# Performance work log

Measured on AMD Instinct MI355X. Metric: run time of the kernel, lower is better.

Reference implementation:

```python
import jax, jax.numpy as jnp
import numpy as np

T, B = 50, 512
S, A, BEL, H, E, M = 256, 32, 1024, 1024, 1024, 256
MIN_STD = 0.1


def setup_inputs() -> dict:
    key = jax.random.key(0)
    ks = jax.random.split(key, 24)
    def rn(k, shape, scale=1.0):
        return jax.random.normal(k, shape, dtype=jnp.float32) * scale
    w = 0.05  # weight init scale
    return {
        "prev_state": rn(ks[0], (B, S)),
        "actions": rn(ks[1], (T, B, A)),
        "prev_belief": rn(ks[2], (B, BEL)),
        "observations": rn(ks[3], (T, B, E)),
        "nonterminals": jnp.ones((T, B, 1), dtype=jnp.float32),
        "map_embeddings": rn(ks[4], (T, B, M)),
        "map_embeddings_post": rn(ks[5], (T, B, M)),
        "noise_prior": rn(ks[6], (T, B, S)),
        "noise_post": rn(ks[7], (T, B, S)),
        "W_sa": rn(ks[8], (BEL, S + A + M), w), "b_sa": jnp.zeros((BEL,), jnp.float32),
        "W_ih": rn(ks[9], (3 * BEL, BEL), w), "b_ih": jnp.zeros((3 * BEL,), jnp.float32),
        "W_hh": rn(ks[10], (3 * BEL, BEL), w), "b_hh": jnp.zeros((3 * BEL,), jnp.float32),
        "W_bp": rn(ks[11], (H, BEL), w), "b_bp": jnp.zeros((H,), jnp.float32),
        "W_sp": rn(ks[12], (2 * S, H), w), "b_sp": jnp.zeros((2 * S,), jnp.float32),
        "W_bq": rn(ks[13], (H, BEL + E + M), w), "b_bq": jnp.zeros((H,), jnp.float32),
        "W_sq": rn(ks[14], (2 * S, H), w), "b_sq": jnp.zeros((2 * S,), jnp.float32),
    }


def reference(prev_state, actions, prev_belief, observations, nonterminals,
              map_embeddings, map_embeddings_post, noise_prior, noise_post,
              W_sa, b_sa, W_ih, b_ih, W_hh, b_hh,
              W_bp, b_bp, W_sp, b_sp, W_bq, b_bq, W_sq, b_sq):
    relu = jax.nn.relu
    def lin(x, W, b):
        return x @ W.T + b

    def gru(x, h):  # torch.nn.GRUCell math
        gi = x @ W_ih.T + b_ih
        gh = h @ W_hh.T + b_hh
        i_r, i_z, i_n = jnp.split(gi, 3, axis=1)
        h_r, h_z, h_n = jnp.split(gh, 3, axis=1)
        r = jax.nn.sigmoid(i_r + h_r)
        z = jax.nn.sigmoid(i_z + h_z)
        n = jnp.tanh(i_n + r * h_n)
        return (1.0 - z) * n + z * h

    def std(raw):
        return jnp.minimum(jax.nn.softplus(raw) + MIN_STD, 5.0)

    def step(carry, xs):
        belief, post_state = carry
        a, obs, nt, me, mp, np_, nq = xs
        s = post_state * nt
        hid = relu(lin(jnp.concatenate([s, a, me], axis=1), W_sa, b_sa))
        belief = gru(hid, belief)
        # prior p(z_t | h_t)
        hp = relu(lin(belief, W_bp, b_bp))
        p_mean, p_raw = jnp.split(lin(hp, W_sp, b_sp), 2, axis=1)
        p_std = std(p_raw)
        p_state = p_mean + p_std * np_
        # posterior q(z_t | h_t, e_t, m_t)
        hq = relu(lin(jnp.concatenate([belief, obs, mp], axis=1), W_bq, b_bq))
        q_mean, q_raw = jnp.split(lin(hq, W_sq, b_sq), 2, axis=1)
        q_std = std(q_raw)
        q_state = q_mean + q_std * nq
        return (belief, q_state), (belief, p_state, p_mean, p_std, q_state, q_mean, q_std)

    _, outs = jax.lax.scan(
        step, (prev_belief, prev_state),
        (actions, observations, nonterminals, map_embeddings,
         map_embeddings_post, noise_prior, noise_post))
    return outs  # 7 arrays, each (T, B, *)
```

## Files before the change

### kernel.cpp

```cpp
#include <hip/hip_runtime.h>
#include <hip/hip_bf16.h>

#define NT 50
#define NB 512
#define SD 256
#define BD 1024
#define HD 1024
#define ED 1024
#define MD 256
#define NBLK 512
#define PGSZ (1024 * 256)
#define K1BIG 0x40000000
#define WPRE_OFF 49152

typedef __attribute__((ext_vector_type(8))) short bf16x8;
typedef __attribute__((ext_vector_type(4))) float f32x4;

__device__ __forceinline__ void gload_lds16(const void* g, void* l) {
  __builtin_amdgcn_global_load_lds(
      (const __attribute__((address_space(1))) void*)g,
      (__attribute__((address_space(3))) void*)l, 16, 0, 0);
}
__device__ __forceinline__ void gload_lds16_sc0(const void* g, void* l) {
  __builtin_amdgcn_global_load_lds(
      (const __attribute__((address_space(1))) void*)g,
      (__attribute__((address_space(3))) void*)l, 16, 0, 1);
}

__device__ __forceinline__ void aload16(const void* a, f32x4* r) {
  asm volatile("global_load_dwordx4 %0, %1, off sc0" : "=&v"(*r) : "v"(a) : "memory");
}
__device__ __forceinline__ void aload4(const void* a, float* r) {
  asm volatile("global_load_dword %0, %1, off sc0" : "=&v"(*r) : "v"(a) : "memory");
}
__device__ __forceinline__ void aload2(const void* a, unsigned* r) {
  asm volatile("global_load_ushort %0, %1, off sc0" : "=&v"(*r) : "v"(a) : "memory");
}
#define VMWAIT(N)                                        \
  asm volatile("s_waitcnt vmcnt(" #N ")" ::: "memory");  \
  __builtin_amdgcn_sched_barrier(0);

__device__ __forceinline__ void astore16(void* g, f32x4 v) {
  asm volatile("global_store_dwordx4 %0, %1, off sc0" :: "v"(g), "v"(v) : "memory");
}
__device__ __forceinline__ void astore4(void* g, float v) {
  asm volatile("global_store_dword %0, %1, off sc0" :: "v"(g), "v"(v) : "memory");
}
__device__ __forceinline__ void astore2(void* g, unsigned v) {
  asm volatile("global_store_short %0, %1, off sc0" :: "v"(g), "v"(v) : "memory");
}
__device__ __forceinline__ void ntstore4(void* g, float v) {
  asm volatile("global_store_dword %0, %1, off nt" :: "v"(g), "v"(v) : "memory");
}

__device__ __forceinline__ float sigmoidf_(float x) { return 1.0f / (1.0f + __expf(-x)); }
__device__ __forceinline__ float softplusf_(float x) {
  return (x > 0.0f) ? (x + log1pf(__expf(-x))) : log1pf(__expf(x));
}
__device__ __forceinline__ unsigned short bfb(float x) {
  __hip_bfloat16 h = __float2bfloat16(x);
  return __builtin_bit_cast(unsigned short, h);
}
__device__ __forceinline__ float b2f(unsigned short u) {
  __hip_bfloat16 h = __builtin_bit_cast(__hip_bfloat16, u);
  return __bfloat162float(h);
}

__device__ __forceinline__ void wpre_issue(const __hip_bfloat16* W, int ldw,
                                           char* lds, int tid) {
  const int w = tid >> 6, lane = tid & 63;
  const __hip_bfloat16* wrow = W + (size_t)lane * ldw;
  char* wpre = lds + WPRE_OFF;
#pragma unroll
  for (int c = 0; c < 3; ++c) {
    gload_lds16(wrow + (c << 6) + (2 * w) * 8, wpre + c * 8192 + (2 * w) * 1024);
    gload_lds16(wrow + (c << 6) + (2 * w + 1) * 8, wpre + c * 8192 + (2 * w + 1) * 1024);
  }
}

__device__ __forceinline__ void xbar_pf(unsigned* cnt, int inst, int xcd, int nx,
                                        const __hip_bfloat16* nextW, int nextLdw,
                                        char* lds, int tid) {
  asm volatile("s_waitcnt vmcnt(0) lgkmcnt(0)" ::: "memory");
  __syncthreads();
  unsigned* c = cnt + 256 + (size_t)(inst * 8 + xcd) * 16;
  if (tid == 0)
    __hip_atomic_fetch_add(c, 1u, __ATOMIC_RELAXED, __HIP_MEMORY_SCOPE_AGENT);
  if (nextW) wpre_issue(nextW, nextLdw, lds, tid);
  if (tid == 0) {
    while (__hip_atomic_load(c, __ATOMIC_RELAXED, __HIP_MEMORY_SCOPE_AGENT) < (unsigned)nx)
      __builtin_amdgcn_s_sleep(2);
  }
  __syncthreads();
}

__device__ __noinline__ void gemm64(
    int EPI, char* lds, bool pre,
    const __hip_bfloat16* __restrict__ A1, int lda1,
    const __hip_bfloat16* __restrict__ A2, int lda2, int K1,
    const __hip_bfloat16* __restrict__ Wr, int ldw, int nIter,
    const float* __restrict__ bias, const void* __restrict__ Cadd,
    __hip_bfloat16* __restrict__ Cb, int ldc, int m0) {
  const int tid = threadIdx.x;
  const int lane = tid & 63, w = tid >> 6;
  const int wr = w >> 1, wc = w & 1;
  f32x4 acc[2][2] = {};
  const __hip_bfloat16* a1r = A1 + (size_t)(m0 + lane) * lda1;
  const __hip_bfloat16* a2r = A2 ? (A2 + (size_t)(m0 + lane) * lda2) : a1r;
  const __hip_bfloat16* wrow = Wr + (size_t)lane * ldw;
  char* wpre = lds + WPRE_OFF;

  auto aissue = [&](int it) {
    const int k0 = it << 6;
    char* la = lds + (size_t)(it % 3) * 16384;
    const __hip_bfloat16* as = (k0 < K1) ? (a1r + k0) : (a2r + (k0 - K1));
    gload_lds16_sc0(as + (2 * w) * 8, la + (2 * w) * 1024);
    gload_lds16_sc0(as + (2 * w + 1) * 8, la + (2 * w + 1) * 1024);
  };
  auto stageAW = [&](int it) {
    const int k0 = it << 6;
    char* la = lds + (size_t)(it % 3) * 16384;
    char* lb = la + 8192;
    const __hip_bfloat16* as = (k0 < K1) ? (a1r + k0) : (a2r + (k0 - K1));
    gload_lds16_sc0(as + (2 * w) * 8, la + (2 * w) * 1024);
    gload_lds16_sc0(as + (2 * w + 1) * 8, la + (2 * w + 1) * 1024);
    gload_lds16(wrow + k0 + (2 * w) * 8, lb + (2 * w) * 1024);
    gload_lds16(wrow + k0 + (2 * w + 1) * 8, lb + (2 * w + 1) * 1024);
  };

  __syncthreads();
  if (!pre) wpre_issue(Wr, ldw, lds, tid);
  aissue(0);
  aissue(1);
  aissue(2);
  VMWAIT(4)
  __builtin_amdgcn_s_barrier();
  __builtin_amdgcn_sched_barrier(0);

  const int kq = lane >> 4, r15 = lane & 15;
  for (int i = 0; i < nIter; ++i) {
    const char* la = lds + (size_t)(i % 3) * 16384;
    const char* lb = (i < 3) ? (wpre + (size_t)i * 8192) : (la + 8192);
#pragma unroll
    for (int s = 0; s < 2; ++s) {
      bf16x8 af[2], bfr[2];
#pragma unroll
      for (int m = 0; m < 2; ++m)
        af[m] = *(const bf16x8*)(la + (size_t)((s * 4 + kq) * 64 + wr * 32 + m * 16 + r15) * 16);
#pragma unroll
      for (int n = 0; n < 2; ++n)
        bfr[n] = *(const bf16x8*)(lb + (size_t)((s * 4 + kq) * 64 + wc * 32 + n * 16 + r15) * 16);
#pragma unroll
      for (int m = 0; m < 2; ++m)
#pragma unroll
        for (int n = 0; n < 2; ++n)
          acc[m][n] = __builtin_amdgcn_mfma_f32_16x16x32_bf16(af[m], bfr[n], acc[m][n], 0, 0, 0);
    }
    if (i + 1 < nIter) {
      if (i == 0) {
        VMWAIT(2)
      } else if (i + 2 < nIter) {
        VMWAIT(4)
      } else {
        VMWAIT(0)
      }
      __builtin_amdgcn_s_barrier();
      __builtin_amdgcn_sched_barrier(0);
      if (i + 3 < nIter) stageAW(i + 3);
    }
  }

  const int rg = lane >> 4;
  unsigned adu[2][2][4];
  if (EPI == 5) {
#pragma unroll
    for (int m = 0; m < 2; ++m)
#pragma unroll
      for (int n = 0; n < 2; ++n) {
        const int col = wc * 32 + n * 16 + r15;
#pragma unroll
        for (int i2 = 0; i2 < 4; ++i2) {
          const int row = m0 + wr * 32 + m * 16 + rg * 4 + i2;
          aload2((const unsigned short*)Cadd + (size_t)row * ldc + col, &adu[m][n][i2]);
        }
      }
    VMWAIT(0)
  }
#pragma unroll
  for (int m = 0; m < 2; ++m) {
#pragma unroll
    for (int n = 0; n < 2; ++n) {
      const int col = wc * 32 + n * 16 + r15;
      const float bv = bias ? bias[col] : 0.0f;
#pragma unroll
      for (int i2 = 0; i2 < 4; ++i2) {
        const int row = m0 + wr * 32 + m * 16 + rg * 4 + i2;
        float v = acc[m][n][i2] + bv;
        if (EPI == 5) v += b2f((unsigned short)adu[m][n][i2]);
        if (EPI != 4) v = v > 0.0f ? v : 0.0f;
        astore2(Cb + (size_t)row * ldc + col, (unsigned)bfb(v));
      }
    }
  }
}

__device__ __noinline__ void gemm_gru(
    char* lds, const __hip_bfloat16* __restrict__ Wih3,
    const __hip_bfloat16* __restrict__ Whh3,
    const float* __restrict__ b_ih, const float* __restrict__ b_hh,
    const __hip_bfloat16* __restrict__ hid, const __hip_bfloat16* __restrict__ belR,
    __hip_bfloat16* __restrict__ belW, float* __restrict__ outT, int n, int m0) {
  const int tid = threadIdx.x;
  const int lane = tid & 63, w = tid >> 6;
  f32x4 agi[3] = {}, agh[3] = {};
  const __hip_bfloat16* hrow = hid + (size_t)(m0 + lane) * BD;
  const __hip_bfloat16* brow = belR + (size_t)(m0 + lane) * BD;
  const int wln = (lane < 48) ? lane : 47;
  const __hip_bfloat16* wirow = Wih3 + (size_t)(n * 48 + wln) * BD;
  const __hip_bfloat16* whrow = Whh3 + (size_t)(n * 48 + wln) * BD;

  auto stage = [&](int it) {
    const int k0 = it << 5;
    char* buf = lds + (size_t)(it % 3) * 16384;
    gload_lds16_sc0(hrow + k0 + w * 8, buf + w * 1024);
    gload_lds16_sc0(brow + k0 + w * 8, buf + 4096 + w * 1024);
    gload_lds16(wirow + k0 + w * 8, buf + 8192 + w * 1024);
    gload_lds16(whrow + k0 + w * 8, buf + 12288 + w * 1024);
  };

  __syncthreads();
  stage(0);
  stage(1);
  VMWAIT(4)
  __builtin_amdgcn_s_barrier();
  __builtin_amdgcn_sched_barrier(0);

  const int kq = lane >> 4, r15 = lane & 15;
  for (int i = 0; i < 32; ++i) {
    if (i + 2 < 32) stage(i + 2);
    const char* buf = lds + (size_t)(i % 3) * 16384;
    bf16x8 ah = *(const bf16x8*)(buf + (size_t)(kq * 64 + w * 16 + r15) * 16);
    bf16x8 ab = *(const bf16x8*)(buf + 4096 + (size_t)(kq * 64 + w * 16 + r15) * 16);
#pragma unroll
    for (int g = 0; g < 3; ++g) {
      bf16x8 wi = *(const bf16x8*)(buf + 8192 + (size_t)(kq * 64 + g * 16 + r15) * 16);
      bf16x8 wh = *(const bf16x8*)(buf + 12288 + (size_t)(kq * 64 + g * 16 + r15) * 16);
      agi[g] = __builtin_amdgcn_mfma_f32_16x16x32_bf16(ah, wi, agi[g], 0, 0, 0);
      agh[g] = __builtin_amdgcn_mfma_f32_16x16x32_bf16(ab, wh, agh[g], 0, 0, 0);
    }
    if (i + 1 < 32) {
      if (i + 2 < 32) {
        VMWAIT(4)
      } else {
        VMWAIT(0)
      }
      __builtin_amdgcn_s_barrier();
      __builtin_amdgcn_sched_barrier(0);
    }
  }

  const int rg = lane >> 4;
  const int unit = n * 16 + r15;
  const int rowb = m0 + w * 16 + rg * 4;
  const float bir = b_ih[unit], biz = b_ih[1024 + unit], bin = b_ih[2048 + unit];
  const float bhr = b_hh[unit], bhz = b_hh[1024 + unit], bhn = b_hh[2048 + unit];
  unsigned hp4[4];
#pragma unroll
  for (int i = 0; i < 4; ++i)
    aload2(belR + (size_t)(rowb + i) * BD + unit, &hp4[i]);
  VMWAIT(0)
#pragma unroll
  for (int i = 0; i < 4; ++i) {
    const int row = rowb + i;
    float r_ = sigmoidf_((agi[0][i] + bir) + (agh[0][i] + bhr));
    float z_ = sigmoidf_((agi[1][i] + biz) + (agh[1][i] + bhz));
    float n_ = tanhf((agi[2][i] + bin) + r_ * (agh[2][i] + bhn));
    float hv = b2f((unsigned short)hp4[i]);
    float bel = (1.0f - z_) * n_ + z_ * hv;
    ntstore4(outT + (size_t)row * BD + unit, bel);
    astore2(belW + (size_t)row * BD + unit, (unsigned)bfb(bel));
  }
}

__device__ __noinline__ void gemm_head64(
    char* lds, bool pre, const __hip_bfloat16* __restrict__ A,
    const __hip_bfloat16* __restrict__ Wr, const float* __restrict__ bias,
    const float* __restrict__ noise, float* __restrict__ st_o, float* __restrict__ mn_o,
    float* __restrict__ sd_o, const float* __restrict__ ntn,
    __hip_bfloat16* __restrict__ sprev, int isq, int n0, int m0) {
  const int tid = threadIdx.x;
  const int lane = tid & 63, w = tid >> 6;
  const int wr = w >> 1, wc = w & 1;
  f32x4 acc[2][2] = {};
  const __hip_bfloat16* ar = A + (size_t)(m0 + lane) * BD;
  const __hip_bfloat16* wrow = Wr + (size_t)lane * BD;
  char* wpre = lds + WPRE_OFF;

  auto aissue = [&](int it) {
    const int k0 = it << 6;
    char* la = lds + (size_t)(it % 3) * 16384;
    gload_lds16_sc0(ar + k0 + (2 * w) * 8, la + (2 * w) * 1024);
    gload_lds16_sc0(ar + k0 + (2 * w + 1) * 8, la + (2 * w + 1) * 1024);
  };
  auto stageAW = [&](int it) {
    const int k0 = it << 6;
    char* la = lds + (size_t)(it % 3) * 16384;
    char* lb = la + 8192;
    gload_lds16_sc0(ar + k0 + (2 * w) * 8, la + (2 * w) * 1024);
    gload_lds16_sc0(ar + k0 + (2 * w + 1) * 8, la + (2 * w + 1) * 1024);
    gload_lds16(wrow + k0 + (2 * w) * 8, lb + (2 * w) * 1024);
    gload_lds16(wrow + k0 + (2 * w + 1) * 8, lb + (2 * w + 1) * 1024);
  };

  __syncthreads();
  if (!pre) wpre_issue(Wr, BD, lds, tid);
  aissue(0);
  aissue(1);
  aissue(2);
  VMWAIT(4)
  __builtin_amdgcn_s_barrier();
  __builtin_amdgcn_sched_barrier(0);

  const int kq = lane >> 4, r15 = lane & 15;
  for (int i = 0; i < 16; ++i) {
    const char* la = lds + (size_t)(i % 3) * 16384;
    const char* lb = (i < 3) ? (wpre + (size_t)i * 8192) : (la + 8192);
#pragma unroll
    for (int s = 0; s < 2; ++s) {
      bf16x8 af[2], bfr[2];
#pragma unroll
      for (int m = 0; m < 2; ++m)
        af[m] = *(const bf16x8*)(la + (size_t)((s * 4 + kq) * 64 + wr * 32 + m * 16 + r15) * 16);
#pragma unroll
      for (int n = 0; n < 2; ++n)
        bfr[n] = *(const bf16x8*)(lb + (size_t)((s * 4 + kq) * 64 + wc * 32 + n * 16 + r15) * 16);
#pragma unroll
      for (int m = 0; m < 2; ++m)
#pragma unroll
        for (int n = 0; n < 2; ++n)
          acc[m][n] = __builtin_amdgcn_mfma_f32_16x16x32_bf16(af[m], bfr[n], acc[m][n], 0, 0, 0);
    }
    if (i + 1 < 16) {
      if (i == 0) {
        VMWAIT(2)
      } else if (i + 2 < 16) {
        VMWAIT(4)
      } else {
        VMWAIT(0)
      }
      __builtin_amdgcn_s_barrier();
      __builtin_amdgcn_sched_barrier(0);
      if (i + 3 < 16) stageAW(i + 3);
    }
  }

  const int rg = lane >> 4;
  const bool even = (r15 & 1) == 0;
#pragma unroll
  for (int m = 0; m < 2; ++m) {
#pragma unroll
    for (int n = 0; n < 2; ++n) {
      const int col = n0 + wc * 32 + n * 16 + r15;
      const int j = col >> 1;
      const float bv = bias[col];
#pragma unroll
      for (int i2 = 0; i2 < 4; ++i2) {
        const int row = m0 + wr * 32 + m * 16 + rg * 4 + i2;
        float v = acc[m][n][i2] + bv;
        float partner = __shfl_xor(v, 1);
        float mean = even ? v : partner;
        float raw = even ? partner : v;
        float sd = fminf(softplusf_(raw) + 0.1f, 5.0f);
        const size_t o = (size_t)row * SD + j;
        if (even) {
          float st = mean + sd * noise[o];
          ntstore4(mn_o + o, mean);
          ntstore4(st_o + o, st);
          if (isq) astore2(sprev + o, (unsigned)bfb(st * ntn[row]));
        } else {
          ntstore4(sd_o + o, sd);
        }
      }
    }
  }
}

struct Args {
  const float *prev_state, *actions, *prev_belief, *observations, *nonterminals,
      *me, *mp, *noise_p, *noise_q,
      *W_sa, *b_sa, *W_ih, *b_ih, *W_hh, *b_hh,
      *W_bp, *b_bp, *W_sp, *b_sp, *W_bq, *b_bq, *W_sq, *b_sq;
  float* out;
  unsigned* cnt;
  __hip_bfloat16 *Wsa, *Wih3, *Whh3, *Wbp, *Wbq, *Wsp, *Wsq;
  __hip_bfloat16 *actme, *obsall, *hqall, *sprev, *belA, *belB, *hid, *hpb, *hqb;
  float *bsp_ro, *bsq_ro;
};

__global__ __launch_bounds__(256) void prep(Args P) {
  const int gtid = blockIdx.x * 256 + threadIdx.x;
  for (int i = gtid; i < BD * 576; i += PGSZ) {
    int r = i / 576, k = i - r * 576;
    P.Wsa[i] = __float2bfloat16(k < 544 ? P.W_sa[(size_t)r * 544 + k] : 0.0f);
  }
  for (int i = gtid; i < 3 * BD * BD; i += PGSZ) {
    int rp = i >> 10, k = i & 1023;
    int n = rp / 48, rem = rp - n * 48, g = rem >> 4, u = rem & 15;
    size_t src = (size_t)(g * 1024 + n * 16 + u) * 1024 + k;
    P.Wih3[i] = __float2bfloat16(P.W_ih[src]);
    P.Whh3[i] = __float2bfloat16(P.W_hh[src]);
  }
  for (int i = gtid; i < HD * BD; i += PGSZ) P.Wbp[i] = __float2bfloat16(P.W_bp[i]);
  for (int i = gtid; i < HD * 2304; i += PGSZ) P.Wbq[i] = __float2bfloat16(P.W_bq[i]);
  for (int i = gtid; i < 512 * HD; i += PGSZ) {
    int r = i >> 10, k = i & 1023;
    int dr = (r < 256) ? (2 * r) : (2 * (r - 256) + 1);
    P.Wsp[(size_t)dr * 1024 + k] = __float2bfloat16(P.W_sp[i]);
    P.Wsq[(size_t)dr * 1024 + k] = __float2bfloat16(P.W_sq[i]);
  }
  for (int i = gtid; i < 512; i += PGSZ) {
    int dr = (i < 256) ? (2 * i) : (2 * (i - 256) + 1);
    P.bsp_ro[dr] = P.b_sp[i];
    P.bsq_ro[dr] = P.b_sq[i];
  }
  for (int i = gtid; i < NT * NB * 320; i += PGSZ) {
    int tb = i / 320, j = i - tb * 320;
    float v = (j < 32) ? P.actions[(size_t)tb * 32 + j]
                       : (j < 288 ? P.me[(size_t)tb * 256 + (j - 32)] : 0.0f);
    P.actme[i] = __float2bfloat16(v);
  }
  for (size_t i = gtid; i < (size_t)NT * NB * 1280; i += PGSZ) {
    size_t tb = i / 1280;
    int j = (int)(i - tb * 1280);
    float v = (j < ED) ? P.observations[tb * ED + j] : P.mp[tb * MD + (j - ED)];
    P.obsall[i] = __float2bfloat16(v);
  }
  for (int i = gtid; i < NB * SD; i += PGSZ) {
    int r = i >> 8;
    P.sprev[i] = __float2bfloat16(P.prev_state[i] * P.nonterminals[r]);
  }
  for (int i = gtid; i < NB * BD; i += PGSZ) P.belA[i] = __float2bfloat16(P.prev_belief[i]);
}

__global__ __launch_bounds__(256, 2) void preg(Args P) {
  __shared__ alignas(16) char lds[73728];
  const int mt = blockIdx.x % 400, nt = blockIdx.x / 400;
  gemm64(4, lds, false, P.obsall, 1280, nullptr, 0, K1BIG,
         P.Wbq + (size_t)nt * 64 * 2304 + 1024, 2304, 20,
         nullptr, nullptr, P.hqall + nt * 64, 1024, mt * 64);
}

__global__ __launch_bounds__(256, 2) void mega(Args P) {
  __shared__ alignas(16) char lds[73728];
  __shared__ int sh[3];
  const int tid = threadIdx.x;

  if (tid == 0) {
    unsigned x;
    asm volatile("s_getreg_b32 %0, hwreg(HW_REG_XCC_ID)" : "=s"(x));
    x &= 7u;
    unsigned s = __hip_atomic_fetch_add(P.cnt + x * 16, 1u, __ATOMIC_RELAXED,
                                        __HIP_MEMORY_SCOPE_AGENT);
    sh[0] = (int)x;
    sh[1] = (int)s;
  }
  __syncthreads();
  const int xcd = sh[0], slot = sh[1];

  if (tid == 0) {
    __hip_atomic_fetch_add(P.cnt + 128, 1u, __ATOMIC_RELAXED, __HIP_MEMORY_SCOPE_AGENT);
    while (__hip_atomic_load(P.cnt + 128, __ATOMIC_RELAXED, __HIP_MEMORY_SCOPE_AGENT) <
           (unsigned)NBLK)
      __builtin_amdgcn_s_sleep(4);
    sh[2] = (int)__hip_atomic_load(P.cnt + xcd * 16, __ATOMIC_RELAXED,
                                   __HIP_MEMORY_SCOPE_AGENT);
  }
  __syncthreads();
  const int nx = sh[2];
  const int m0 = xcd * 64;
  const size_t o_ps = (size_t)NT * NB * BD;
  const size_t blk = (size_t)NT * NB * SD;

  const __hip_bfloat16* wA = (slot < 16) ? P.Wsa + (size_t)slot * 64 * 576 : nullptr;
  const int lA = 576;
  const __hip_bfloat16* wD = nullptr; int lD = 0;
  if (slot < 16) { wD = P.Wbp + (size_t)slot * 64 * BD; lD = BD; }
  else if (slot < 32) { wD = P.Wbq + (size_t)(slot - 16) * 64 * 2304; lD = 2304; }
  const __hip_bfloat16* wE = nullptr; int lE = 0;
  if (slot < 8) { wE = P.Wsp + (size_t)slot * 64 * BD; lE = BD; }
  else if (slot < 16) { wE = P.Wsq + (size_t)(slot - 8) * 64 * BD; lE = BD; }

  if (wA) wpre_issue(wA, lA, lds, tid);

  for (int t = 0; t < NT; ++t) {
    const int inst = t * 4;
    const __hip_bfloat16* belR = (t & 1) ? P.belB : P.belA;
    __hip_bfloat16* belW = (t & 1) ? P.belA : P.belB;
    for (int tt = slot; tt < 16; tt += nx) {
      gemm64(1, lds, tt == slot, P.sprev, SD, P.actme + (size_t)t * NB * 320, 320, 256,
             P.Wsa + (size_t)tt * 64 * 576, 576, 9,
             P.b_sa + tt * 64, nullptr, P.hid + tt * 64, BD, m0);
    }
    xbar_pf(P.cnt, inst + 0, xcd, nx, nullptr, 0, lds, tid);
    for (int tt = slot; tt < 64; tt += nx) {
      gemm_gru(lds, P.Wih3, P.Whh3, P.b_ih, P.b_hh, P.hid, belR, belW,
               P.out + (size_t)t * NB * BD, tt, m0);
    }
    xbar_pf(P.cnt, inst + 1, xcd, nx, wD, lD, lds, tid);
    for (int tt = slot; tt < 32; tt += nx) {
      const bool pre = (tt == slot);
      if (tt < 16) {
        gemm64(1, lds, pre, belW, BD, nullptr, 0, K1BIG,
               P.Wbp + (size_t)tt * 64 * BD, BD, 16,
               P.b_bp + tt * 64, nullptr, P.hpb + tt * 64, HD, m0);
      } else {
        const int n = tt - 16;
        gemm64(5, lds, pre, belW, BD, nullptr, 0, K1BIG,
               P.Wbq + (size_t)n * 64 * 2304, 2304, 16,
               P.b_bq + n * 64, P.hqall + (size_t)t * NB * HD + n * 64,
               P.hqb + n * 64, HD, m0);
      }
    }
    xbar_pf(P.cnt, inst + 2, xcd, nx, wE, lE, lds, tid);
    {
      const float* ntn = P.nonterminals + (size_t)((t + 1 < NT) ? t + 1 : t) * NB;
      const size_t to = (size_t)t * NB * SD;
      for (int tt = slot; tt < 16; tt += nx) {
        const bool pre = (tt == slot);
        if (tt < 8)
          gemm_head64(lds, pre, P.hpb, P.Wsp + (size_t)tt * 64 * BD, P.bsp_ro,
                      P.noise_p + to, P.out + o_ps + to, P.out + o_ps + blk + to,
                      P.out + o_ps + 2 * blk + to, ntn, P.sprev, 0, tt * 64, m0);
        else
          gemm_head64(lds, pre, P.hqb, P.Wsq + (size_t)(tt - 8) * 64 * BD, P.bsq_ro,
                      P.noise_q + to, P.out + o_ps + 3 * blk + to,
                      P.out + o_ps + 4 * blk + to, P.out + o_ps + 5 * blk + to,
                      ntn, P.sprev, 1, (tt - 8) * 64, m0);
      }
    }
    xbar_pf(P.cnt, inst + 3, xcd, nx, wA, lA, lds, tid);
  }
}


extern "C" void kernel_launch(void* const* d_in, const int* in_sizes, int n_in,
                              void* d_out, int out_size, void* d_ws, size_t ws_size,
                              hipStream_t stream) {
  Args P;
  P.prev_state = (const float*)d_in[0];
  P.actions = (const float*)d_in[1];
  P.prev_belief = (const float*)d_in[2];
  P.observations = (const float*)d_in[3];
  P.nonterminals = (const float*)d_in[4];
  P.me = (const float*)d_in[5];
  P.mp = (const float*)d_in[6];
  P.noise_p = (const float*)d_in[7];
  P.noise_q = (const float*)d_in[8];
  P.W_sa = (const float*)d_in[9];  P.b_sa = (const float*)d_in[10];
  P.W_ih = (const float*)d_in[11]; P.b_ih = (const float*)d_in[12];
  P.W_hh = (const float*)d_in[13]; P.b_hh = (const float*)d_in[14];
  P.W_bp = (const float*)d_in[15]; P.b_bp = (const float*)d_in[16];
  P.W_sp = (const float*)d_in[17]; P.b_sp = (const float*)d_in[18];
  P.W_bq = (const float*)d_in[19]; P.b_bq = (const float*)d_in[20];
  P.W_sq = (const float*)d_in[21]; P.b_sq = (const float*)d_in[22];
  P.out = (float*)d_out;

  char* p = (char*)d_ws;
  auto carve = [&](size_t bytes) -> char* {
    char* r = p;
    p += (bytes + 255) & ~(size_t)255;
    return r;
  };
  const size_t cnt_bytes = (size_t)65536 * 4;
  P.cnt = (unsigned*)carve(cnt_bytes);
  P.Wsa = (__hip_bfloat16*)carve((size_t)BD * 576 * 2);
  P.Wih3 = (__hip_bfloat16*)carve((size_t)3 * BD * BD * 2);
  P.Whh3 = (__hip_bfloat16*)carve((size_t)3 * BD * BD * 2);
  P.Wbp = (__hip_bfloat16*)carve((size_t)HD * BD * 2);
  P.Wbq = (__hip_bfloat16*)carve((size_t)HD * 2304 * 2);
  P.Wsp = (__hip_bfloat16*)carve((size_t)512 * HD * 2);
  P.Wsq = (__hip_bfloat16*)carve((size_t)512 * HD * 2);
  P.bsp_ro = (float*)carve(512 * 4);
  P.bsq_ro = (float*)carve(512 * 4);
  P.actme = (__hip_bfloat16*)carve((size_t)NT * NB * 320 * 2);
  P.obsall = (__hip_bfloat16*)carve((size_t)NT * NB * 1280 * 2);
  P.hqall = (__hip_bfloat16*)carve((size_t)NT * NB * HD * 2);
  P.sprev = (__hip_bfloat16*)carve((size_t)NB * SD * 2);
  P.belA = (__hip_bfloat16*)carve((size_t)NB * BD * 2);
  P.belB = (__hip_bfloat16*)carve((size_t)NB * BD * 2);
  P.hid = (__hip_bfloat16*)carve((size_t)NB * BD * 2);
  P.hpb = (__hip_bfloat16*)carve((size_t)NB * HD * 2);
  P.hqb = (__hip_bfloat16*)carve((size_t)NB * HD * 2);

  hipMemsetAsync(P.cnt, 0, cnt_bytes, stream);
  prep<<<1024, 256, 0, stream>>>(P);
  preg<<<6400, 256, 0, stream>>>(P);
  mega<<<NBLK, 256, 0, stream>>>(P);
}
```

Baseline: 5.379 ms.

## Replace cross-barrier weight prefetch with deeper K=32 multi-stage LDS pipelines

```diff
diff --git a/kernel.cpp b/kernel.cpp
--- a/kernel.cpp
+++ b/kernel.cpp
@@ -11,7 +11,6 @@
 #define NBLK 512
 #define PGSZ (1024 * 256)
 #define K1BIG 0x40000000
-#define WPRE_OFF 49152
 
 typedef __attribute__((ext_vector_type(8))) short bf16x8;
 typedef __attribute__((ext_vector_type(4))) float f32x4;
@@ -27,12 +26,6 @@
       (__attribute__((address_space(3))) void*)l, 16, 0, 1);
 }
 
-__device__ __forceinline__ void aload16(const void* a, f32x4* r) {
-  asm volatile("global_load_dwordx4 %0, %1, off sc0" : "=&v"(*r) : "v"(a) : "memory");
-}
-__device__ __forceinline__ void aload4(const void* a, float* r) {
-  asm volatile("global_load_dword %0, %1, off sc0" : "=&v"(*r) : "v"(a) : "memory");
-}
 __device__ __forceinline__ void aload2(const void* a, unsigned* r) {
   asm volatile("global_load_ushort %0, %1, off sc0" : "=&v"(*r) : "v"(a) : "memory");
 }
@@ -40,12 +33,6 @@
   asm volatile("s_waitcnt vmcnt(" #N ")" ::: "memory");  \
   __builtin_amdgcn_sched_barrier(0);
 
-__device__ __forceinline__ void astore16(void* g, f32x4 v) {
-  asm volatile("global_store_dwordx4 %0, %1, off sc0" :: "v"(g), "v"(v) : "memory");
-}
-__device__ __forceinline__ void astore4(void* g, float v) {
-  asm volatile("global_store_dword %0, %1, off sc0" :: "v"(g), "v"(v) : "memory");
-}
 __device__ __forceinline__ void astore2(void* g, unsigned v) {
   asm volatile("global_store_short %0, %1, off sc0" :: "v"(g), "v"(v) : "memory");
 }
@@ -66,28 +53,20 @@
   return __bfloat162float(h);
 }
 
-__device__ __forceinline__ void wpre_issue(const __hip_bfloat16* W, int ldw,
-                                           char* lds, int tid) {
-  const int w = tid >> 6, lane = tid & 63;
-  const __hip_bfloat16* wrow = W + (size_t)lane * ldw;
-  char* wpre = lds + WPRE_OFF;
-#pragma unroll
-  for (int c = 0; c < 3; ++c) {
-    gload_lds16(wrow + (c << 6) + (2 * w) * 8, wpre + c * 8192 + (2 * w) * 1024);
-    gload_lds16(wrow + (c << 6) + (2 * w + 1) * 8, wpre + c * 8192 + (2 * w + 1) * 1024);
-  }
-}
-
-__device__ __forceinline__ void xbar_pf(unsigned* cnt, int inst, int xcd, int nx,
-                                        const __hip_bfloat16* nextW, int nextLdw,
-                                        char* lds, int tid) {
+__device__ __forceinline__ void wait_rem(int rem) {
+  if (rem >= 4) { VMWAIT(8) }
+  else if (rem == 3) { VMWAIT(6) }
+  else if (rem == 2) { VMWAIT(4) }
+  else if (rem == 1) { VMWAIT(2) }
+  else { VMWAIT(0) }
+}
+
+__device__ __forceinline__ void xbar(unsigned* cnt, int inst, int xcd, int nx) {
   asm volatile("s_waitcnt vmcnt(0) lgkmcnt(0)" ::: "memory");
   __syncthreads();
-  unsigned* c = cnt + 256 + (size_t)(inst * 8 + xcd) * 16;
-  if (tid == 0)
+  if (threadIdx.x == 0) {
+    unsigned* c = cnt + 256 + (size_t)(inst * 8 + xcd) * 16;
     __hip_atomic_fetch_add(c, 1u, __ATOMIC_RELAXED, __HIP_MEMORY_SCOPE_AGENT);
-  if (nextW) wpre_issue(nextW, nextLdw, lds, tid);
-  if (tid == 0) {
     while (__hip_atomic_load(c, __ATOMIC_RELAXED, __HIP_MEMORY_SCOPE_AGENT) < (unsigned)nx)
       __builtin_amdgcn_s_sleep(2);
   }
@@ -95,7 +74,7 @@
 }
 
 __device__ __noinline__ void gemm64(
-    int EPI, char* lds, bool pre,
+    int EPI, char* lds,
     const __hip_bfloat16* __restrict__ A1, int lda1,
     const __hip_bfloat16* __restrict__ A2, int lda2, int K1,
     const __hip_bfloat16* __restrict__ Wr, int ldw, int nIter,
@@ -108,65 +87,43 @@
   const __hip_bfloat16* a1r = A1 + (size_t)(m0 + lane) * lda1;
   const __hip_bfloat16* a2r = A2 ? (A2 + (size_t)(m0 + lane) * lda2) : a1r;
   const __hip_bfloat16* wrow = Wr + (size_t)lane * ldw;
-  char* wpre = lds + WPRE_OFF;
-
-  auto aissue = [&](int it) {
-    const int k0 = it << 6;
-    char* la = lds + (size_t)(it % 3) * 16384;
+
+  auto stage = [&](int it) {
+    const int k0 = it << 5;
+    char* la = lds + (size_t)(it % 6) * 8192;
     const __hip_bfloat16* as = (k0 < K1) ? (a1r + k0) : (a2r + (k0 - K1));
-    gload_lds16_sc0(as + (2 * w) * 8, la + (2 * w) * 1024);
-    gload_lds16_sc0(as + (2 * w + 1) * 8, la + (2 * w + 1) * 1024);
+    gload_lds16_sc0(as + w * 8, la + w * 1024);
+    gload_lds16(wrow + k0 + w * 8, la + 4096 + w * 1024);
   };
-  auto stageAW = [&](int it) {
-    const int k0 = it << 6;
-    char* la = lds + (size_t)(it % 3) * 16384;
-    char* lb = la + 8192;
-    const __hip_bfloat16* as = (k0 < K1) ? (a1r + k0) : (a2r + (k0 - K1));
-    gload_lds16_sc0(as + (2 * w) * 8, la + (2 * w) * 1024);
-    gload_lds16_sc0(as + (2 * w + 1) * 8, la + (2 * w + 1) * 1024);
-    gload_lds16(wrow + k0 + (2 * w) * 8, lb + (2 * w) * 1024);
-    gload_lds16(wrow + k0 + (2 * w + 1) * 8, lb + (2 * w + 1) * 1024);
-  };
-
-  __syncthreads();
-  if (!pre) wpre_issue(Wr, ldw, lds, tid);
-  aissue(0);
-  aissue(1);
-  aissue(2);
-  VMWAIT(4)
+
+  __syncthreads();
+#pragma unroll
+  for (int s = 0; s < 5; ++s) stage(s);
+  VMWAIT(8)
   __builtin_amdgcn_s_barrier();
   __builtin_amdgcn_sched_barrier(0);
 
   const int kq = lane >> 4, r15 = lane & 15;
   for (int i = 0; i < nIter; ++i) {
-    const char* la = lds + (size_t)(i % 3) * 16384;
-    const char* lb = (i < 3) ? (wpre + (size_t)i * 8192) : (la + 8192);
-#pragma unroll
-    for (int s = 0; s < 2; ++s) {
-      bf16x8 af[2], bfr[2];
-#pragma unroll
-      for (int m = 0; m < 2; ++m)
-        af[m] = *(const bf16x8*)(la + (size_t)((s * 4 + kq) * 64 + wr * 32 + m * 16 + r15) * 16);
+    if (i + 5 < nIter) stage(i + 5);
+    const char* la = lds + (size_t)(i % 6) * 8192;
+    bf16x8 af[2], bfr[2];
+#pragma unroll
+    for (int m = 0; m < 2; ++m)
+      af[m] = *(const bf16x8*)(la + (size_t)(kq * 64 + wr * 32 + m * 16 + r15) * 16);
+#pragma unroll
+    for (int n = 0; n < 2; ++n)
+      bfr[n] = *(const bf16x8*)(la + 4096 + (size_t)(kq * 64 + wc * 32 + n * 16 + r15) * 16);
+#pragma unroll
+    for (int m = 0; m < 2; ++m)
 #pragma unroll
       for (int n = 0; n < 2; ++n)
-        bfr[n] = *(const bf16x8*)(lb + (size_t)((s * 4 + kq) * 64 + wc * 32 + n * 16 + r15) * 16);
-#pragma unroll
-      for (int m = 0; m < 2; ++m)
-#pragma unroll
-        for (int n = 0; n < 2; ++n)
-          acc[m][n] = __builtin_amdgcn_mfma_f32_16x16x32_bf16(af[m], bfr[n], acc[m][n], 0, 0, 0);
-    }
+        acc[m][n] = __builtin_amdgcn_mfma_f32_16x16x32_bf16(af[m], bfr[n], acc[m][n], 0, 0, 0);
     if (i + 1 < nIter) {
-      if (i == 0) {
-        VMWAIT(2)
-      } else if (i + 2 < nIter) {
-        VMWAIT(4)
-      } else {
-        VMWAIT(0)
-      }
+      const int last = (i + 5 < nIter) ? i + 5 : nIter - 1;
+      wait_rem(last - (i + 1));
       __builtin_amdgcn_s_barrier();
       __builtin_amdgcn_sched_barrier(0);
-      if (i + 3 < nIter) stageAW(i + 3);
     }
   }
 
@@ -221,7 +178,7 @@
 
   auto stage = [&](int it) {
     const int k0 = it << 5;
-    char* buf = lds + (size_t)(it % 3) * 16384;
+    char* buf = lds + (size_t)(it % 4) * 16384;
     gload_lds16_sc0(hrow + k0 + w * 8, buf + w * 1024);
     gload_lds16_sc0(brow + k0 + w * 8, buf + 4096 + w * 1024);
     gload_lds16(wirow + k0 + w * 8, buf + 8192 + w * 1024);
@@ -231,14 +188,15 @@
   __syncthreads();
   stage(0);
   stage(1);
-  VMWAIT(4)
+  stage(2);
+  VMWAIT(8)
   __builtin_amdgcn_s_barrier();
   __builtin_amdgcn_sched_barrier(0);
 
   const int kq = lane >> 4, r15 = lane & 15;
   for (int i = 0; i < 32; ++i) {
-    if (i + 2 < 32) stage(i + 2);
-    const char* buf = lds + (size_t)(i % 3) * 16384;
+    if (i + 3 < 32) stage(i + 3);
+    const char* buf = lds + (size_t)(i % 4) * 16384;
     bf16x8 ah = *(const bf16x8*)(buf + (size_t)(kq * 64 + w * 16 + r15) * 16);
     bf16x8 ab = *(const bf16x8*)(buf + 4096 + (size_t)(kq * 64 + w * 16 + r15) * 16);
 #pragma unroll
@@ -249,11 +207,11 @@
       agh[g] = __builtin_amdgcn_mfma_f32_16x16x32_bf16(ab, wh, agh[g], 0, 0, 0);
     }
     if (i + 1 < 32) {
-      if (i + 2 < 32) {
-        VMWAIT(4)
-      } else {
-        VMWAIT(0)
-      }
+      const int last = (i + 3 < 32) ? i + 3 : 31;
+      const int rem = last - (i + 1);
+      if (rem >= 2) { VMWAIT(8) }
+      else if (rem == 1) { VMWAIT(4) }
+      else { VMWAIT(0) }
       __builtin_amdgcn_s_barrier();
       __builtin_amdgcn_sched_barrier(0);
     }
@@ -283,7 +241,7 @@
 }
 
 __device__ __noinline__ void gemm_head64(
-    char* lds, bool pre, const __hip_bfloat16* __restrict__ A,
+    char* lds, const __hip_bfloat16* __restrict__ A,
     const __hip_bfloat16* __restrict__ Wr, const float* __restrict__ bias,
     const float* __restrict__ noise, float* __restrict__ st_o, float* __restrict__ mn_o,
     float* __restrict__ sd_o, const float* __restrict__ ntn,
@@ -294,63 +252,42 @@
   f32x4 acc[2][2] = {};
   const __hip_bfloat16* ar = A + (size_t)(m0 + lane) * BD;
   const __hip_bfloat16* wrow = Wr + (size_t)lane * BD;
-  char* wpre = lds + WPRE_OFF;
-
-  auto aissue = [&](int it) {
-    const int k0 = it << 6;
-    char* la = lds + (size_t)(it % 3) * 16384;
-    gload_lds16_sc0(ar + k0 + (2 * w) * 8, la + (2 * w) * 1024);
-    gload_lds16_sc0(ar + k0 + (2 * w + 1) * 8, la + (2 * w + 1) * 1024);
+
+  auto stage = [&](int it) {
+    const int k0 = it << 5;
+    char* la = lds + (size_t)(it % 6) * 8192;
+    gload_lds16_sc0(ar + k0 + w * 8, la + w * 1024);
+    gload_lds16(wrow + k0 + w * 8, la + 4096 + w * 1024);
   };
-  auto stageAW = [&](int it) {
-    const int k0 = it << 6;
-    char* la = lds + (size_t)(it % 3) * 16384;
-    char* lb = la + 8192;
-    gload_lds16_sc0(ar + k0 + (2 * w) * 8, la + (2 * w) * 1024);
-    gload_lds16_sc0(ar + k0 + (2 * w + 1) * 8, la + (2 * w + 1) * 1024);
-    gload_lds16(wrow + k0 + (2 * w) * 8, lb + (2 * w) * 1024);
-    gload_lds16(wrow + k0 + (2 * w + 1) * 8, lb + (2 * w + 1) * 1024);
-  };
-
-  __syncthreads();
-  if (!pre) wpre_issue(Wr, BD, lds, tid);
-  aissue(0);
-  aissue(1);
-  aissue(2);
-  VMWAIT(4)
+
+  __syncthreads();
+#pragma unroll
+  for (int s = 0; s < 5; ++s) stage(s);
+  VMWAIT(8)
   __builtin_amdgcn_s_barrier();
   __builtin_amdgcn_sched_barrier(0);
 
   const int kq = lane >> 4, r15 = lane & 15;
-  for (int i = 0; i < 16; ++i) {
-    const char* la = lds + (size_t)(i % 3) * 16384;
-    const char* lb = (i < 3) ? (wpre + (size_t)i * 8192) : (la + 8192);
-#pragma unroll
-    for (int s = 0; s < 2; ++s) {
-      bf16x8 af[2], bfr[2];
-#pragma unroll
-      for (int m = 0; m < 2; ++m)
-        af[m] = *(const bf16x8*)(la + (size_t)((s * 4 + kq) * 64 + wr * 32 + m * 16 + r15) * 16);
+  for (int i = 0; i < 32; ++i) {
+    if (i + 5 < 32) stage(i + 5);
+    const char* la = lds + (size_t)(i % 6) * 8192;
+    bf16x8 af[2], bfr[2];
+#pragma unroll
+    for (int m = 0; m < 2; ++m)
+      af[m] = *(const bf16x8*)(la + (size_t)(kq * 64 + wr * 32 + m * 16 + r15) * 16);
+#pragma unroll
+    for (int n = 0; n < 2; ++n)
+      bfr[n] = *(const bf16x8*)(la + 4096 + (size_t)(kq * 64 + wc * 32 + n * 16 + r15) * 16);
+#pragma unroll
+    for (int m = 0; m < 2; ++m)
 #pragma unroll
       for (int n = 0; n < 2; ++n)
-        bfr[n] = *(const bf16x8*)(lb + (size_t)((s * 4 + kq) * 64 + wc * 32 + n * 16 + r15) * 16);
-#pragma unroll
-      for (int m = 0; m < 2; ++m)
-#pragma unroll
-        for (int n = 0; n < 2; ++n)
-          acc[m][n] = __builtin_amdgcn_mfma_f32_16x16x32_bf16(af[m], bfr[n], acc[m][n], 0, 0, 0);
-    }
-    if (i + 1 < 16) {
-      if (i == 0) {
-        VMWAIT(2)
-      } else if (i + 2 < 16) {
-        VMWAIT(4)
-      } else {
-        VMWAIT(0)
-      }
+        acc[m][n] = __builtin_amdgcn_mfma_f32_16x16x32_bf16(af[m], bfr[n], acc[m][n], 0, 0, 0);
+    if (i + 1 < 32) {
+      const int last = (i + 5 < 32) ? i + 5 : 31;
+      wait_rem(last - (i + 1));
       __builtin_amdgcn_s_barrier();
       __builtin_amdgcn_sched_barrier(0);
-      if (i + 3 < 16) stageAW(i + 3);
     }
   }
 
@@ -443,15 +380,15 @@
 }
 
 __global__ __launch_bounds__(256, 2) void preg(Args P) {
-  __shared__ alignas(16) char lds[73728];
+  __shared__ alignas(16) char lds[65536];
   const int mt = blockIdx.x % 400, nt = blockIdx.x / 400;
-  gemm64(4, lds, false, P.obsall, 1280, nullptr, 0, K1BIG,
-         P.Wbq + (size_t)nt * 64 * 2304 + 1024, 2304, 20,
+  gemm64(4, lds, P.obsall, 1280, nullptr, 0, K1BIG,
+         P.Wbq + (size_t)nt * 64 * 2304 + 1024, 2304, 40,
          nullptr, nullptr, P.hqall + nt * 64, 1024, mt * 64);
 }
 
 __global__ __launch_bounds__(256, 2) void mega(Args P) {
-  __shared__ alignas(16) char lds[73728];
+  __shared__ alignas(16) char lds[65536];
   __shared__ int sh[3];
   const int tid = threadIdx.x;
 
@@ -481,64 +418,51 @@
   const size_t o_ps = (size_t)NT * NB * BD;
   const size_t blk = (size_t)NT * NB * SD;
 
-  const __hip_bfloat16* wA = (slot < 16) ? P.Wsa + (size_t)slot * 64 * 576 : nullptr;
-  const int lA = 576;
-  const __hip_bfloat16* wD = nullptr; int lD = 0;
-  if (slot < 16) { wD = P.Wbp + (size_t)slot * 64 * BD; lD = BD; }
-  else if (slot < 32) { wD = P.Wbq + (size_t)(slot - 16) * 64 * 2304; lD = 2304; }
-  const __hip_bfloat16* wE = nullptr; int lE = 0;
-  if (slot < 8) { wE = P.Wsp + (size_t)slot * 64 * BD; lE = BD; }
-  else if (slot < 16) { wE = P.Wsq + (size_t)(slot - 8) * 64 * BD; lE = BD; }
-
-  if (wA) wpre_issue(wA, lA, lds, tid);
-
   for (int t = 0; t < NT; ++t) {
     const int inst = t * 4;
     const __hip_bfloat16* belR = (t & 1) ? P.belB : P.belA;
     __hip_bfloat16* belW = (t & 1) ? P.belA : P.belB;
     for (int tt = slot; tt < 16; tt += nx) {
-      gemm64(1, lds, tt == slot, P.sprev, SD, P.actme + (size_t)t * NB * 320, 320, 256,
-             P.Wsa + (size_t)tt * 64 * 576, 576, 9,
+      gemm64(1, lds, P.sprev, SD, P.actme + (size_t)t * NB * 320, 320, 256,
+             P.Wsa + (size_t)tt * 64 * 576, 576, 18,
              P.b_sa + tt * 64, nullptr, P.hid + tt * 64, BD, m0);
     }
-    xbar_pf(P.cnt, inst + 0, xcd, nx, nullptr, 0, lds, tid);
+    xbar(P.cnt, inst + 0, xcd, nx);
     for (int tt = slot; tt < 64; tt += nx) {
       gemm_gru(lds, P.Wih3, P.Whh3, P.b_ih, P.b_hh, P.hid, belR, belW,
                P.out + (size_t)t * NB * BD, tt, m0);
     }
-    xbar_pf(P.cnt, inst + 1, xcd, nx, wD, lD, lds, tid);
+    xbar(P.cnt, inst + 1, xcd, nx);
     for (int tt = slot; tt < 32; tt += nx) {
-      const bool pre = (tt == slot);
       if (tt < 16) {
-        gemm64(1, lds, pre, belW, BD, nullptr, 0, K1BIG,
-               P.Wbp + (size_t)tt * 64 * BD, BD, 16,
+        gemm64(1, lds, belW, BD, nullptr, 0, K1BIG,
+               P.Wbp + (size_t)tt * 64 * BD, BD, 32,
                P.b_bp + tt * 64, nullptr, P.hpb + tt * 64, HD, m0);
       } else {
         const int n = tt - 16;
-        gemm64(5, lds, pre, belW, BD, nullptr, 0, K1BIG,
-               P.Wbq + (size_t)n * 64 * 2304, 2304, 16,
+        gemm64(5, lds, belW, BD, nullptr, 0, K1BIG,
+               P.Wbq + (size_t)n * 64 * 2304, 2304, 32,
                P.b_bq + n * 64, P.hqall + (size_t)t * NB * HD + n * 64,
                P.hqb + n * 64, HD, m0);
       }
     }
-    xbar_pf(P.cnt, inst + 2, xcd, nx, wE, lE, lds, tid);
+    xbar(P.cnt, inst + 2, xcd, nx);
     {
       const float* ntn = P.nonterminals + (size_t)((t + 1 < NT) ? t + 1 : t) * NB;
       const size_t to = (size_t)t * NB * SD;
       for (int tt = slot; tt < 16; tt += nx) {
-        const bool pre = (tt == slot);
         if (tt < 8)
-          gemm_head64(lds, pre, P.hpb, P.Wsp + (size_t)tt * 64 * BD, P.bsp_ro,
+          gemm_head64(lds, P.hpb, P.Wsp + (size_t)tt * 64 * BD, P.bsp_ro,
                       P.noise_p + to, P.out + o_ps + to, P.out + o_ps + blk + to,
                       P.out + o_ps + 2 * blk + to, ntn, P.sprev, 0, tt * 64, m0);
         else
-          gemm_head64(lds, pre, P.hqb, P.Wsq + (size_t)(tt - 8) * 64 * BD, P.bsq_ro,
+          gemm_head64(lds, P.hqb, P.Wsq + (size_t)(tt - 8) * 64 * BD, P.bsq_ro,
                       P.noise_q + to, P.out + o_ps + 3 * blk + to,
                       P.out + o_ps + 4 * blk + to, P.out + o_ps + 5 * blk + to,
                       ntn, P.sprev, 1, (tt - 8) * 64, m0);
       }
     }
-    xbar_pf(P.cnt, inst + 3, xcd, nx, wA, lA, lds, tid);
+    xbar(P.cnt, inst + 3, xcd, nx);
   }
 }
 
```

Measured after the change: 5.749 ms. 1.07x slower.
